# Kernel optimization log

Hardware: AMD Instinct MI355X
Metric: run time of the kernel (lower is better)

Reference implementation:

```python
import jax, jax.numpy as jnp
import numpy as np

NUM_RELS = 64
EDGES_PER_REL = 16384
N_NODES = 100000
IN_FEAT = 128
OUT_FEAT = 128
NUM_BASES = 16
E = NUM_RELS * EDGES_PER_REL


def setup_inputs() -> dict:
    key = jax.random.key(0)
    ks = jax.random.split(key, 8)
    feat = jax.random.normal(ks[0], (N_NODES, IN_FEAT), dtype=jnp.float32)
    weight = jax.random.normal(ks[1], (NUM_BASES, IN_FEAT, OUT_FEAT), dtype=jnp.float32) * 0.05
    w_comp = jax.random.normal(ks[2], (NUM_RELS, NUM_BASES), dtype=jnp.float32) * 0.3
    h_bias = jnp.zeros((OUT_FEAT,), dtype=jnp.float32)
    loop_weight = jax.random.normal(ks[3], (IN_FEAT, OUT_FEAT), dtype=jnp.float32) * 0.05
    norm = jax.random.uniform(ks[4], (E, 1), dtype=jnp.float32)
    src = jax.random.randint(ks[5], (E,), 0, N_NODES, dtype=jnp.int32).astype(jnp.int64)
    dst = jax.random.randint(ks[6], (E,), 0, N_NODES, dtype=jnp.int32).astype(jnp.int64)
    # edges are sorted by relation type with uniform per-relation sections
    etypes = jnp.repeat(jnp.arange(NUM_RELS, dtype=jnp.int64), EDGES_PER_REL)
    return {"feat": feat, "weight": weight, "w_comp": w_comp, "h_bias": h_bias,
            "loop_weight": loop_weight, "norm": norm, "src": src, "dst": dst,
            "etypes": etypes, "section": EDGES_PER_REL}


def reference(feat, weight, w_comp, h_bias, loop_weight, norm, src, dst, etypes, section):
    num_rels, num_bases = w_comp.shape
    n_nodes, in_feat = feat.shape
    out_feat = weight.shape[2]
    # basis composition: per-relation weights [R, in, out]
    W = jnp.matmul(w_comp, weight.reshape(num_bases, in_feat * out_feat))
    W = W.reshape(num_rels, in_feat, out_feat)
    # gather per-edge source features (edges sorted by relation, uniform sections)
    h_e = feat[src]                                   # [E, in]
    n_edges = h_e.shape[0]
    h_r = h_e.reshape(num_rels, section, in_feat)     # [R, e_r, in]
    msg = jnp.einsum('rei,rio->reo', h_r, W)          # grouped matmul
    msg = msg.reshape(n_edges, out_feat) * norm       # edge-norm scaling
    # scatter-sum aggregation to destination nodes
    node_repr = jax.ops.segment_sum(msg, dst, num_segments=n_nodes)
    node_repr = node_repr + h_bias + jnp.matmul(feat, loop_weight)
    return jax.nn.relu(node_repr)
```

## Files before the change

### kernel.cpp

```cpp
#include <hip/hip_runtime.h>

#define N_NODES 100000
#define N_PAD 100352
#define NBLK 392
#define IN_FEAT 128
#define OUT_FEAT 128
#define NUM_RELS 64
#define EDGES_PER_REL 16384
#define NUM_BASES 16
#define E_TOTAL (NUM_RELS * EDGES_PER_REL)

typedef __bf16 bf16x8 __attribute__((ext_vector_type(8)));
typedef float floatx4 __attribute__((ext_vector_type(4)));

__global__ __launch_bounds__(256) void compose_all_bf16_kernel(
    const float* __restrict__ weight, const float* __restrict__ w_comp,
    const float* __restrict__ loop_w, __bf16* __restrict__ Wp,
    __bf16* __restrict__ Lp) {
  int gid = blockIdx.x * 256 + threadIdx.x;
  if (gid < NUM_RELS * 16384) {
    int r = gid >> 14;
    int off = gid & 16383;
    int j = off & 7, n = (off >> 3) & 127, kp = off >> 10;
    int k = kp * 8 + j;
    const float* wc = w_comp + r * NUM_BASES;
    float acc = 0.f;
#pragma unroll
    for (int b = 0; b < NUM_BASES; ++b)
      acc += wc[b] * weight[b * 16384 + k * 128 + n];
    Wp[gid] = (__bf16)acc;
  } else {
    int idx = gid - NUM_RELS * 16384;
    int j = idx & 7, n = (idx >> 3) & 127, kp = idx >> 10;
    Lp[idx] = (__bf16)loop_w[(kp * 8 + j) * 128 + n];
  }
}

__global__ __launch_bounds__(256) void compose_w_f32_kernel(
    const float* __restrict__ weight, const float* __restrict__ w_comp,
    float* __restrict__ W) {
  int idx = blockIdx.x * 256 + threadIdx.x;
  int r = idx >> 14;
  int io = idx & 16383;
  const float* wc = w_comp + r * NUM_BASES;
  float acc = 0.f;
#pragma unroll
  for (int b = 0; b < NUM_BASES; ++b)
    acc += wc[b] * weight[b * 16384 + io];
  W[idx] = acc;
}

__global__ __launch_bounds__(256) void init_out_mfma(
    const float* __restrict__ feat, __bf16* __restrict__ featb,
    const __bf16* __restrict__ Lp, const float* __restrict__ bias,
    float* __restrict__ out) {
  __shared__ __bf16 A_lds[64 * 136];
  int t = threadIdx.x;
  long base = (long)blockIdx.x * 64;
#pragma unroll
  for (int j = 0; j < 8; ++j) {
    int idx = t + j * 256;
    int e = idx >> 5, k4 = idx & 31;
    long n = base + e;
    float4 v = make_float4(0.f, 0.f, 0.f, 0.f);
    bool ok = (n < N_NODES);
    if (ok) v = ((const float4*)feat)[n * 32 + k4];
    __bf16 tb[4] = {(__bf16)v.x, (__bf16)v.y, (__bf16)v.z, (__bf16)v.w};
    *(ushort4*)&A_lds[e * 136 + k4 * 4] = *(ushort4*)tb;
    if (featb && ok)
      *(ushort4*)(featb + n * 128 + k4 * 4) = *(ushort4*)tb;
  }
  __syncthreads();

  int wave = t >> 6, lane = t & 63;
  int m16 = lane & 15, quad = lane >> 4;
  floatx4 acc[8];
#pragma unroll
  for (int nt = 0; nt < 8; ++nt) acc[nt] = (floatx4){0.f, 0.f, 0.f, 0.f};

  const __bf16* a_base = &A_lds[(wave * 16 + m16) * 136 + quad * 8];
#pragma unroll
  for (int ks = 0; ks < 4; ++ks) {
    bf16x8 a = *(const bf16x8*)(a_base + ks * 32);
    int kp = ks * 4 + quad;
#pragma unroll
    for (int nt = 0; nt < 8; ++nt) {
      bf16x8 b = *(const bf16x8*)(Lp + (kp * 128 + nt * 16 + m16) * 8);
      acc[nt] = __builtin_amdgcn_mfma_f32_16x16x32_bf16(a, b, acc[nt], 0, 0, 0);
    }
  }

  float bv[8];
#pragma unroll
  for (int nt = 0; nt < 8; ++nt) bv[nt] = bias[nt * 16 + m16];
#pragma unroll
  for (int r = 0; r < 4; ++r) {
    long n = base + wave * 16 + quad * 4 + r;
    if (n < N_NODES) {
#pragma unroll
      for (int nt = 0; nt < 8; ++nt)
        out[n * 128 + nt * 16 + m16] = acc[nt][r] + bv[nt];
    }
  }
}

__global__ __launch_bounds__(256) void zero_kernel(int* __restrict__ p) {
  p[blockIdx.x * 256 + threadIdx.x] = 0;
}

__global__ __launch_bounds__(256) void hist8_kernel(
    const int* __restrict__ dst, int* __restrict__ cnt8, int cshift) {
  int e = blockIdx.x * 256 + threadIdx.x;
  int c = e >> cshift;
  atomicAdd(&cnt8[c * N_PAD + dst[e]], 1);
}

__global__ __launch_bounds__(256) void scan1_kernel(
    const int* __restrict__ cnt, int* __restrict__ row,
    int* __restrict__ bsum) {
  __shared__ int s[256];
  int t = threadIdx.x;
  int idx = blockIdx.x * 256 + t;
  int v = cnt[idx];
  s[t] = v;
  __syncthreads();
  for (int o = 1; o < 256; o <<= 1) {
    int x = (t >= o) ? s[t - o] : 0;
    __syncthreads();
    s[t] += x;
    __syncthreads();
  }
  row[idx] = s[t] - v;
  if (t == 255) bsum[blockIdx.x] = s[t];
}

__global__ __launch_bounds__(512) void scan2_kernel(
    const int* __restrict__ bsum, int* __restrict__ boff) {
  __shared__ int s[512];
  int t = threadIdx.x;
  int v = (t < NBLK) ? bsum[blockIdx.x * NBLK + t] : 0;
  s[t] = v;
  __syncthreads();
  for (int o = 1; o < 512; o <<= 1) {
    int x = (t >= o) ? s[t - o] : 0;
    __syncthreads();
    s[t] += x;
    __syncthreads();
  }
  if (t < NBLK) boff[blockIdx.x * NBLK + t] = s[t] - v;
}

__global__ __launch_bounds__(256) void scan3_kernel(
    int* __restrict__ row, const int* __restrict__ boff,
    int* __restrict__ fill) {
  int idx = blockIdx.x * 256 + threadIdx.x;
  int v = row[idx] + boff[blockIdx.x];
  row[idx] = v;
  fill[idx] = v;
}

__global__ __launch_bounds__(256) void scatter_pos_kernel(
    const int* __restrict__ dst, int* __restrict__ fill8,
    int* __restrict__ pos, int cshift) {
  int e = blockIdx.x * 256 + threadIdx.x;
  int c = e >> cshift;
  pos[e] = atomicAdd(&fill8[c * N_PAD + dst[e]], 1);
}

__global__ __launch_bounds__(256) void edge_gemm_mfma(
    const float* __restrict__ feat, const __bf16* __restrict__ featb,
    const __bf16* __restrict__ Wp, const float* __restrict__ norm,
    const int* __restrict__ src, const int* __restrict__ pos,
    unsigned short* __restrict__ msg, int e_lo) {
  __shared__ __bf16 B_lds[IN_FEAT * OUT_FEAT];
  __shared__ int s_pos[64];
  int t = threadIdx.x;
  long base = (long)e_lo + (long)blockIdx.x * 64;
  int rel = (int)(base >> 14);
  const __bf16* Wr = Wp + (long)rel * (IN_FEAT * OUT_FEAT);

  if (t < 64) s_pos[t] = pos[base + t];

  {
    const uint4* Wr4 = (const uint4*)Wr;
    uint4* B4 = (uint4*)B_lds;
#pragma unroll
    for (int j = 0; j < 8; ++j) B4[t + j * 256] = Wr4[t + j * 256];
  }

  int wave = t >> 6, lane = t & 63;
  int m16 = lane & 15, quad = lane >> 4;

  int srow = src[base + wave * 16 + m16];
  bf16x8 a[4];
  if (featb) {
    const __bf16* ap = featb + (long)srow * 128 + quad * 8;
#pragma unroll
    for (int ks = 0; ks < 4; ++ks) a[ks] = *(const bf16x8*)(ap + ks * 32);
  } else {
    const float* fp = feat + (long)srow * 128 + quad * 8;
#pragma unroll
    for (int ks = 0; ks < 4; ++ks) {
      float4 lo = *(const float4*)(fp + ks * 32);
      float4 hi = *(const float4*)(fp + ks * 32 + 4);
      __bf16 tb[8] = {(__bf16)lo.x, (__bf16)lo.y, (__bf16)lo.z, (__bf16)lo.w,
                      (__bf16)hi.x, (__bf16)hi.y, (__bf16)hi.z, (__bf16)hi.w};
      a[ks] = *(bf16x8*)tb;
    }
  }
  float nm[4];
#pragma unroll
  for (int r = 0; r < 4; ++r)
    nm[r] = norm[base + wave * 16 + quad * 4 + r];

  __syncthreads();

  floatx4 acc[8];
#pragma unroll
  for (int nt = 0; nt < 8; ++nt) acc[nt] = (floatx4){0.f, 0.f, 0.f, 0.f};
#pragma unroll
  for (int ks = 0; ks < 4; ++ks) {
    int kp = ks * 4 + quad;
#pragma unroll
    for (int nt = 0; nt < 8; ++nt) {
      bf16x8 b = *(const bf16x8*)(B_lds + (kp * 128 + nt * 16 + m16) * 8);
      acc[nt] = __builtin_amdgcn_mfma_f32_16x16x32_bf16(a[ks], b, acc[nt], 0, 0, 0);
    }
  }

  __syncthreads();
#pragma unroll
  for (int r = 0; r < 4; ++r) {
    int erow = wave * 16 + quad * 4 + r;
#pragma unroll
    for (int nt = 0; nt < 8; ++nt)
      B_lds[erow * 136 + nt * 16 + m16] = (__bf16)(acc[nt][r] * nm[r]);
  }
  __syncthreads();
#pragma unroll
  for (int it = 0; it < 4; ++it) {
    int idx = it * 256 + t;
    int row = idx >> 4, seg = idx & 15;
    uint4 v = *(const uint4*)&B_lds[row * 136 + seg * 8];
    *(uint4*)(msg + (long)s_pos[row] * 128 + seg * 8) = v;
  }
}

__global__ __launch_bounds__(256) void gather_csr_kernel(
    const unsigned short* __restrict__ msg, const int* __restrict__ rowc,
    float* __restrict__ out, int do_relu) {
  int wave = threadIdx.x >> 6, lane = threadIdx.x & 63;
  int n = blockIdx.x * 4 + wave;
  if (n >= N_NODES) return;
  int beg = rowc[n], end = rowc[n + 1];
  if (!do_relu && beg == end) return;
  int half = lane >> 5;
  int c4 = lane & 31;
  float s0 = 0.f, s1 = 0.f, s2 = 0.f, s3 = 0.f;
  for (int j = beg + half; j < end; j += 2) {
    uint2 m = *(const uint2*)(msg + (long)j * 128 + c4 * 4);
    s0 += __uint_as_float(m.x << 16);
    s1 += __uint_as_float(m.x & 0xFFFF0000u);
    s2 += __uint_as_float(m.y << 16);
    s3 += __uint_as_float(m.y & 0xFFFF0000u);
  }
  s0 += __shfl_down(s0, 32);
  s1 += __shfl_down(s1, 32);
  s2 += __shfl_down(s2, 32);
  s3 += __shfl_down(s3, 32);
  if (half == 0) {
    float4 o = ((float4*)out)[(long)n * 32 + c4];
    o.x += s0; o.y += s1; o.z += s2; o.w += s3;
    if (do_relu) {
      o.x = fmaxf(o.x, 0.f); o.y = fmaxf(o.y, 0.f);
      o.z = fmaxf(o.z, 0.f); o.w = fmaxf(o.w, 0.f);
    }
    ((float4*)out)[(long)n * 32 + c4] = o;
  }
}

__global__ __launch_bounds__(256) void init_out_f32_kernel(
    const float* __restrict__ feat, const float* __restrict__ loop_w,
    const float* __restrict__ bias, float* __restrict__ out) {
  __shared__ float4 A4[64][32];
  int t = threadIdx.x;
  long base = (long)blockIdx.x * 64;
#pragma unroll
  for (int j = 0; j < 8; ++j) {
    int idx = t + j * 256;
    int e = idx >> 5, k4 = idx & 31;
    long n = base + e;
    float4 v = make_float4(0.f, 0.f, 0.f, 0.f);
    if (n < N_NODES) v = ((const float4*)feat)[n * 32 + k4];
    A4[e][k4] = v;
  }
  __syncthreads();
  int og = t & 31, eg = t >> 5;
  float acc[8][4];
#pragma unroll
  for (int j = 0; j < 8; ++j)
#pragma unroll
    for (int d = 0; d < 4; ++d) acc[j][d] = 0.f;
  const float4* W4 = (const float4*)loop_w;
  for (int k4 = 0; k4 < 32; ++k4) {
    float4 a[8];
#pragma unroll
    for (int j = 0; j < 8; ++j) a[j] = A4[eg * 8 + j][k4];
#pragma unroll
    for (int d = 0; d < 4; ++d) {
      float4 w = W4[(k4 * 4 + d) * 32 + og];
#pragma unroll
      for (int j = 0; j < 8; ++j) {
        float av = ((const float*)&a[j])[d];
        acc[j][0] += av * w.x;
        acc[j][1] += av * w.y;
        acc[j][2] += av * w.z;
        acc[j][3] += av * w.w;
      }
    }
  }
  float4 b = ((const float4*)bias)[og];
#pragma unroll
  for (int j = 0; j < 8; ++j) {
    long n = base + eg * 8 + j;
    if (n < N_NODES) {
      float4 v = make_float4(acc[j][0] + b.x, acc[j][1] + b.y,
                             acc[j][2] + b.z, acc[j][3] + b.w);
      ((float4*)out)[n * 32 + og] = v;
    }
  }
}

__global__ __launch_bounds__(256) void edge_msg_atomic_kernel(
    const float* __restrict__ feat, const float* __restrict__ W,
    const float* __restrict__ norm, const int* __restrict__ src,
    const int* __restrict__ dst, float* __restrict__ out) {
  __shared__ float4 A4[64][32];
  __shared__ int s_src[64];
  __shared__ int s_dst[64];
  __shared__ float s_norm[64];
  int t = threadIdx.x;
  long base = (long)blockIdx.x * 64;
  int rel = blockIdx.x >> 8;
  const float4* Wr4 = (const float4*)(W + (long)rel * IN_FEAT * OUT_FEAT);
  if (t < 64) {
    s_src[t] = src[base + t];
    s_dst[t] = dst[base + t];
    s_norm[t] = norm[base + t];
  }
  __syncthreads();
#pragma unroll
  for (int j = 0; j < 8; ++j) {
    int idx = t + j * 256;
    int e = idx >> 5, k4 = idx & 31;
    A4[e][k4] = ((const float4*)feat)[(long)s_src[e] * 32 + k4];
  }
  __syncthreads();
  int og = t & 31, eg = t >> 5;
  float acc[8][4];
#pragma unroll
  for (int j = 0; j < 8; ++j)
#pragma unroll
    for (int d = 0; d < 4; ++d) acc[j][d] = 0.f;
  for (int k4 = 0; k4 < 32; ++k4) {
    float4 a[8];
#pragma unroll
    for (int j = 0; j < 8; ++j) a[j] = A4[eg * 8 + j][k4];
#pragma unroll
    for (int d = 0; d < 4; ++d) {
      float4 w = Wr4[(k4 * 4 + d) * 32 + og];
#pragma unroll
      for (int j = 0; j < 8; ++j) {
        float av = ((const float*)&a[j])[d];
        acc[j][0] += av * w.x;
        acc[j][1] += av * w.y;
        acc[j][2] += av * w.z;
        acc[j][3] += av * w.w;
      }
    }
  }
#pragma unroll
  for (int j = 0; j < 8; ++j) {
    int e = eg * 8 + j;
    float nm = s_norm[e];
    float* orow = out + (long)s_dst[e] * OUT_FEAT + og * 4;
#pragma unroll
    for (int d = 0; d < 4; ++d) atomicAdd(orow + d, acc[j][d] * nm);
  }
}

__global__ __launch_bounds__(256) void relu_kernel(float* __restrict__ out) {
  int idx = blockIdx.x * 256 + threadIdx.x;
  float4 v = ((const float4*)out)[idx];
  v.x = fmaxf(v.x, 0.f);
  v.y = fmaxf(v.y, 0.f);
  v.z = fmaxf(v.z, 0.f);
  v.w = fmaxf(v.w, 0.f);
  ((float4*)out)[idx] = v;
}

extern "C" void kernel_launch(void* const* d_in, const int* in_sizes, int n_in,
                              void* d_out, int out_size, void* d_ws, size_t ws_size,
                              hipStream_t stream) {
  const float* feat   = (const float*)d_in[0];
  const float* weight = (const float*)d_in[1];
  const float* w_comp = (const float*)d_in[2];
  const float* h_bias = (const float*)d_in[3];
  const float* loop_w = (const float*)d_in[4];
  const float* norm   = (const float*)d_in[5];
  const int*   src    = (const int*)d_in[6];
  const int*   dst    = (const int*)d_in[7];
  float* out = (float*)d_out;

  const size_t SZ_WP  = (size_t)NUM_RELS * IN_FEAT * OUT_FEAT * 2;
  const size_t SZ_LP  = (size_t)IN_FEAT * OUT_FEAT * 2;
  const size_t SZ_FB  = (size_t)N_NODES * IN_FEAT * 2;
  const size_t SZ_POS = (size_t)E_TOTAL * 4;

  int CH = 0, FB = 0;
  {
    const int chs[10] = {64, 32, 32, 16, 16, 8, 8, 4, 4, 0};
    const int fbs[10] = { 1,  1,  0,  1,  0, 1, 0, 1, 0, 0};
    for (int i = 0; i < 9 && CH == 0; ++i) {
      int ch = chs[i], fb = fbs[i], nc = NUM_RELS / ch;
      size_t need = SZ_WP + SZ_LP + (fb ? SZ_FB : 0) + SZ_POS +
                    2 * (size_t)nc * N_PAD * 4 + 2 * (size_t)nc * NBLK * 4 +
                    (size_t)ch * EDGES_PER_REL * OUT_FEAT * 2;
      if (ws_size >= need) { CH = ch; FB = fb; }
    }
  }

  if (CH > 0) {
    const int NC = NUM_RELS / CH;
    const int chunk_edges = CH * EDGES_PER_REL;
    int cshift = 14;
    for (int x = CH; x > 1; x >>= 1) ++cshift;

    char* p = (char*)d_ws;
    __bf16* Wp = (__bf16*)p;                  p += SZ_WP;
    __bf16* Lp = (__bf16*)p;                  p += SZ_LP;
    __bf16* featb = nullptr;
    if (FB) { featb = (__bf16*)p;             p += SZ_FB; }
    int* pos  = (int*)p;                      p += SZ_POS;
    int* cnt8 = (int*)p;                      p += (size_t)NC * N_PAD * 4;
    int* row8 = (int*)p;                      p += (size_t)NC * N_PAD * 4;
    int* bsum = (int*)p;                      p += (size_t)NC * NBLK * 4;
    int* boff = (int*)p;                      p += (size_t)NC * NBLK * 4;
    unsigned short* msg = (unsigned short*)p;

    hipLaunchKernelGGL(compose_all_bf16_kernel,
                       dim3((NUM_RELS * 16384 + 16384) / 256), dim3(256), 0,
                       stream, weight, w_comp, loop_w, Wp, Lp);
    hipLaunchKernelGGL(init_out_mfma, dim3((N_NODES + 63) / 64), dim3(256), 0,
                       stream, feat, featb, Lp, h_bias, out);
    hipLaunchKernelGGL(zero_kernel, dim3(NC * NBLK), dim3(256), 0, stream, cnt8);
    hipLaunchKernelGGL(hist8_kernel, dim3(E_TOTAL / 256), dim3(256), 0, stream,
                       dst, cnt8, cshift);
    hipLaunchKernelGGL(scan1_kernel, dim3(NC * NBLK), dim3(256), 0, stream,
                       cnt8, row8, bsum);
    hipLaunchKernelGGL(scan2_kernel, dim3(NC), dim3(512), 0, stream, bsum, boff);
    hipLaunchKernelGGL(scan3_kernel, dim3(NC * NBLK), dim3(256), 0, stream,
                       row8, boff, cnt8);
    hipLaunchKernelGGL(scatter_pos_kernel, dim3(E_TOTAL / 256), dim3(256), 0,
                       stream, dst, cnt8, pos, cshift);

    for (int c = 0; c < NC; ++c) {
      hipLaunchKernelGGL(edge_gemm_mfma, dim3(chunk_edges / 64), dim3(256), 0,
                         stream, feat, featb, Wp, norm, src, pos, msg,
                         c * chunk_edges);
      hipLaunchKernelGGL(gather_csr_kernel, dim3((N_NODES + 3) / 4), dim3(256),
                         0, stream, msg, row8 + (size_t)c * N_PAD, out,
                         (c == NC - 1) ? 1 : 0);
    }
  } else {
    float* W = (float*)d_ws;
    hipLaunchKernelGGL(init_out_f32_kernel, dim3((N_NODES + 63) / 64),
                       dim3(256), 0, stream, feat, loop_w, h_bias, out);
    hipLaunchKernelGGL(compose_w_f32_kernel, dim3(NUM_RELS * 16384 / 256),
                       dim3(256), 0, stream, weight, w_comp, W);
    hipLaunchKernelGGL(edge_msg_atomic_kernel, dim3(E_TOTAL / 64), dim3(256), 0,
                       stream, feat, W, norm, src, dst, out);
    hipLaunchKernelGGL(relu_kernel, dim3((N_NODES * OUT_FEAT / 4) / 256),
                       dim3(256), 0, stream, out);
  }
}
```

Measured before the change: 428.8 us.

## Process four edge tiles per block with double-buffered loads; widen gather reads

```diff
diff --git a/kernel.cpp b/kernel.cpp
--- a/kernel.cpp
+++ b/kernel.cpp
@@ -9,6 +9,7 @@
 #define EDGES_PER_REL 16384
 #define NUM_BASES 16
 #define E_TOTAL (NUM_RELS * EDGES_PER_REL)
+#define TPB 4
 
 typedef __bf16 bf16x8 __attribute__((ext_vector_type(8)));
 typedef float floatx4 __attribute__((ext_vector_type(4)));
@@ -173,13 +174,11 @@
     const int* __restrict__ src, const int* __restrict__ pos,
     unsigned short* __restrict__ msg, int e_lo) {
   __shared__ __bf16 B_lds[IN_FEAT * OUT_FEAT];
-  __shared__ int s_pos[64];
+  __shared__ __bf16 D_lds[64 * 136];
   int t = threadIdx.x;
-  long base = (long)e_lo + (long)blockIdx.x * 64;
+  long base = (long)e_lo + (long)blockIdx.x * (64 * TPB);
   int rel = (int)(base >> 14);
   const __bf16* Wr = Wp + (long)rel * (IN_FEAT * OUT_FEAT);
-
-  if (t < 64) s_pos[t] = pos[base + t];
 
   {
     const uint4* Wr4 = (const uint4*)Wr;
@@ -191,59 +190,85 @@
   int wave = t >> 6, lane = t & 63;
   int m16 = lane & 15, quad = lane >> 4;
 
-  int srow = src[base + wave * 16 + m16];
-  bf16x8 a[4];
-  if (featb) {
-    const __bf16* ap = featb + (long)srow * 128 + quad * 8;
-#pragma unroll
-    for (int ks = 0; ks < 4; ++ks) a[ks] = *(const bf16x8*)(ap + ks * 32);
-  } else {
-    const float* fp = feat + (long)srow * 128 + quad * 8;
-#pragma unroll
-    for (int ks = 0; ks < 4; ++ks) {
-      float4 lo = *(const float4*)(fp + ks * 32);
-      float4 hi = *(const float4*)(fp + ks * 32 + 4);
-      __bf16 tb[8] = {(__bf16)lo.x, (__bf16)lo.y, (__bf16)lo.z, (__bf16)lo.w,
-                      (__bf16)hi.x, (__bf16)hi.y, (__bf16)hi.z, (__bf16)hi.w};
-      a[ks] = *(bf16x8*)tb;
-    }
-  }
-  float nm[4];
-#pragma unroll
-  for (int r = 0; r < 4; ++r)
-    nm[r] = norm[base + wave * 16 + quad * 4 + r];
-
-  __syncthreads();
-
-  floatx4 acc[8];
-#pragma unroll
-  for (int nt = 0; nt < 8; ++nt) acc[nt] = (floatx4){0.f, 0.f, 0.f, 0.f};
-#pragma unroll
-  for (int ks = 0; ks < 4; ++ks) {
-    int kp = ks * 4 + quad;
-#pragma unroll
-    for (int nt = 0; nt < 8; ++nt) {
-      bf16x8 b = *(const bf16x8*)(B_lds + (kp * 128 + nt * 16 + m16) * 8);
-      acc[nt] = __builtin_amdgcn_mfma_f32_16x16x32_bf16(a[ks], b, acc[nt], 0, 0, 0);
-    }
-  }
-
-  __syncthreads();
-#pragma unroll
-  for (int r = 0; r < 4; ++r) {
-    int erow = wave * 16 + quad * 4 + r;
-#pragma unroll
-    for (int nt = 0; nt < 8; ++nt)
-      B_lds[erow * 136 + nt * 16 + m16] = (__bf16)(acc[nt][r] * nm[r]);
-  }
-  __syncthreads();
-#pragma unroll
-  for (int it = 0; it < 4; ++it) {
-    int idx = it * 256 + t;
-    int row = idx >> 4, seg = idx & 15;
-    uint4 v = *(const uint4*)&B_lds[row * 136 + seg * 8];
-    *(uint4*)(msg + (long)s_pos[row] * 128 + seg * 8) = v;
-  }
+  bf16x8 aA[4], aB[4];
+  float nmA[4], nmB[4];
+  int poA[4], poB[4];
+  int srow0, srow1;
+
+#define LOAD_SROW(dst, it) (dst) = src[base + (it) * 64 + wave * 16 + m16]
+
+#define LOAD_TILE(aX, nmX, poX, it, srowX)                                   \
+  do {                                                                       \
+    if (featb) {                                                             \
+      const __bf16* ap = featb + (long)(srowX)*128 + quad * 8;               \
+      _Pragma("unroll") for (int ks = 0; ks < 4; ++ks)                       \
+          aX[ks] = *(const bf16x8*)(ap + ks * 32);                           \
+    } else {                                                                 \
+      const float* fp = feat + (long)(srowX)*128 + quad * 8;                 \
+      _Pragma("unroll") for (int ks = 0; ks < 4; ++ks) {                     \
+        float4 lo = *(const float4*)(fp + ks * 32);                          \
+        float4 hi = *(const float4*)(fp + ks * 32 + 4);                      \
+        __bf16 tb[8] = {(__bf16)lo.x, (__bf16)lo.y, (__bf16)lo.z,            \
+                        (__bf16)lo.w, (__bf16)hi.x, (__bf16)hi.y,            \
+                        (__bf16)hi.z, (__bf16)hi.w};                         \
+        aX[ks] = *(bf16x8*)tb;                                               \
+      }                                                                      \
+    }                                                                        \
+    _Pragma("unroll") for (int r = 0; r < 4; ++r)                            \
+        nmX[r] = norm[base + (it) * 64 + wave * 16 + quad * 4 + r];          \
+    _Pragma("unroll") for (int i = 0; i < 4; ++i)                            \
+        poX[i] = pos[base + (it) * 64 + wave * 16 + i * 4 + quad];           \
+  } while (0)
+
+#define COMPUTE_TILE(aX, nmX, poX)                                           \
+  do {                                                                       \
+    floatx4 acc[8];                                                          \
+    _Pragma("unroll") for (int nt = 0; nt < 8; ++nt)                         \
+        acc[nt] = (floatx4){0.f, 0.f, 0.f, 0.f};                             \
+    _Pragma("unroll") for (int ks = 0; ks < 4; ++ks) {                       \
+      int kp = ks * 4 + quad;                                                \
+      _Pragma("unroll") for (int nt = 0; nt < 8; ++nt) {                     \
+        bf16x8 b = *(const bf16x8*)(B_lds + (kp * 128 + nt * 16 + m16) * 8); \
+        acc[nt] =                                                            \
+            __builtin_amdgcn_mfma_f32_16x16x32_bf16(aX[ks], b, acc[nt],      \
+                                                    0, 0, 0);                \
+      }                                                                      \
+    }                                                                        \
+    _Pragma("unroll") for (int r = 0; r < 4; ++r) {                          \
+      int erow = wave * 16 + quad * 4 + r;                                   \
+      _Pragma("unroll") for (int nt = 0; nt < 8; ++nt)                       \
+          D_lds[erow * 136 + nt * 16 + m16] = (__bf16)(acc[nt][r] * nmX[r]); \
+    }                                                                        \
+    __builtin_amdgcn_wave_barrier();                                         \
+    _Pragma("unroll") for (int i = 0; i < 4; ++i) {                          \
+      int row = wave * 16 + i * 4 + quad;                                    \
+      uint4 v = *(const uint4*)&D_lds[row * 136 + m16 * 8];                  \
+      *(uint4*)(msg + (long)poX[i] * 128 + m16 * 8) = v;                     \
+    }                                                                        \
+    __builtin_amdgcn_wave_barrier();                                         \
+  } while (0)
+
+  LOAD_SROW(srow0, 0);
+  LOAD_SROW(srow1, 1);
+  LOAD_TILE(aA, nmA, poA, 0, srow0);
+  __syncthreads();
+
+  LOAD_TILE(aB, nmB, poB, 1, srow1);
+  LOAD_SROW(srow0, 2);
+  COMPUTE_TILE(aA, nmA, poA);
+
+  LOAD_TILE(aA, nmA, poA, 2, srow0);
+  LOAD_SROW(srow1, 3);
+  COMPUTE_TILE(aB, nmB, poB);
+
+  LOAD_TILE(aB, nmB, poB, 3, srow1);
+  COMPUTE_TILE(aA, nmA, poA);
+
+  COMPUTE_TILE(aB, nmB, poB);
+
+#undef LOAD_SROW
+#undef LOAD_TILE
+#undef COMPUTE_TILE
 }
 
 __global__ __launch_bounds__(256) void gather_csr_kernel(
@@ -254,28 +279,41 @@
   if (n >= N_NODES) return;
   int beg = rowc[n], end = rowc[n + 1];
   if (!do_relu && beg == end) return;
-  int half = lane >> 5;
-  int c4 = lane & 31;
-  float s0 = 0.f, s1 = 0.f, s2 = 0.f, s3 = 0.f;
-  for (int j = beg + half; j < end; j += 2) {
-    uint2 m = *(const uint2*)(msg + (long)j * 128 + c4 * 4);
-    s0 += __uint_as_float(m.x << 16);
-    s1 += __uint_as_float(m.x & 0xFFFF0000u);
-    s2 += __uint_as_float(m.y << 16);
-    s3 += __uint_as_float(m.y & 0xFFFF0000u);
-  }
-  s0 += __shfl_down(s0, 32);
-  s1 += __shfl_down(s1, 32);
-  s2 += __shfl_down(s2, 32);
-  s3 += __shfl_down(s3, 32);
-  if (half == 0) {
-    float4 o = ((float4*)out)[(long)n * 32 + c4];
-    o.x += s0; o.y += s1; o.z += s2; o.w += s3;
+  int q = lane >> 4;
+  int c8 = lane & 15;
+  float s[8] = {0.f, 0.f, 0.f, 0.f, 0.f, 0.f, 0.f, 0.f};
+  for (int j = beg; j < end; j += 4) {
+    int jr = j + q;
+    if (jr < end) {
+      uint4 m = *(const uint4*)(msg + (long)jr * 128 + c8 * 8);
+      s[0] += __uint_as_float(m.x << 16);
+      s[1] += __uint_as_float(m.x & 0xFFFF0000u);
+      s[2] += __uint_as_float(m.y << 16);
+      s[3] += __uint_as_float(m.y & 0xFFFF0000u);
+      s[4] += __uint_as_float(m.z << 16);
+      s[5] += __uint_as_float(m.z & 0xFFFF0000u);
+      s[6] += __uint_as_float(m.w << 16);
+      s[7] += __uint_as_float(m.w & 0xFFFF0000u);
+    }
+  }
+#pragma unroll
+  for (int k = 0; k < 8; ++k) {
+    s[k] += __shfl_xor(s[k], 16);
+    s[k] += __shfl_xor(s[k], 32);
+  }
+  if (q == 0) {
+    float4 o0 = ((float4*)out)[(long)n * 32 + c8 * 2];
+    float4 o1 = ((float4*)out)[(long)n * 32 + c8 * 2 + 1];
+    o0.x += s[0]; o0.y += s[1]; o0.z += s[2]; o0.w += s[3];
+    o1.x += s[4]; o1.y += s[5]; o1.z += s[6]; o1.w += s[7];
     if (do_relu) {
-      o.x = fmaxf(o.x, 0.f); o.y = fmaxf(o.y, 0.f);
-      o.z = fmaxf(o.z, 0.f); o.w = fmaxf(o.w, 0.f);
-    }
-    ((float4*)out)[(long)n * 32 + c4] = o;
+      o0.x = fmaxf(o0.x, 0.f); o0.y = fmaxf(o0.y, 0.f);
+      o0.z = fmaxf(o0.z, 0.f); o0.w = fmaxf(o0.w, 0.f);
+      o1.x = fmaxf(o1.x, 0.f); o1.y = fmaxf(o1.y, 0.f);
+      o1.z = fmaxf(o1.z, 0.f); o1.w = fmaxf(o1.w, 0.f);
+    }
+    ((float4*)out)[(long)n * 32 + c8 * 2] = o0;
+    ((float4*)out)[(long)n * 32 + c8 * 2 + 1] = o1;
   }
 }
 
@@ -465,9 +503,9 @@
                        stream, dst, cnt8, pos, cshift);
 
     for (int c = 0; c < NC; ++c) {
-      hipLaunchKernelGGL(edge_gemm_mfma, dim3(chunk_edges / 64), dim3(256), 0,
-                         stream, feat, featb, Wp, norm, src, pos, msg,
-                         c * chunk_edges);
+      hipLaunchKernelGGL(edge_gemm_mfma, dim3(chunk_edges / (64 * TPB)),
+                         dim3(256), 0, stream, feat, featb, Wp, norm, src, pos,
+                         msg, c * chunk_edges);
       hipLaunchKernelGGL(gather_csr_kernel, dim3((N_NODES + 3) / 4), dim3(256),
                          0, stream, msg, row8 + (size_t)c * N_PAD, out,
                          (c == NC - 1) ? 1 : 0);
```

Result: no change. 421.8 us (-1.6%).
